# Kernel optimization log

Measured on AMD Instinct MI355X. Metric: run time of the kernel, lower is better.

Reference implementation:

```python
import jax, jax.numpy as jnp
import numpy as np

B = 256       # decode batch
V = 50257     # per-model vocab size (GPT-2-class)
U = 65536     # union vocab size
M = 3         # number of ensembled models


def setup_inputs() -> dict:
    key = jax.random.key(0)
    ks = jax.random.split(key, 7)
    d = {}
    for i in range(M):
        d[f"logits{i}"] = jax.random.normal(ks[i], (B, V), dtype=jnp.float32)
    for i in range(M):
        # vocab_to_token_id mapping: model-local vocab index -> union vocab index
        d[f"map{i}"] = jax.random.randint(ks[M + i], (V,), 0, U, dtype=jnp.int32)
    d["weights"] = jnp.array([0.4, 0.35, 0.25], dtype=jnp.float32)
    return d


def reference(logits0, logits1, logits2, map0, map1, map2, weights):
    # union_probs[b, map_m[j]] += w_m * softmax(logits_m)[b, j]
    union = jnp.zeros((logits0.shape[0], U), dtype=logits0.dtype)
    for m, (lg, mp) in enumerate(zip((logits0, logits1, logits2),
                                     (map0, map1, map2))):
        p = jax.nn.softmax(lg, axis=-1)          # [B, V]
        union = union.at[:, mp].add(weights[m] * p)  # weighted scatter-add into [B, U]
    return union
```

## Files before the change

kernel.cpp:

```cpp
#include <hip/hip_runtime.h>

#define BB 256
#define VV 50257
#define UU 65536
#define MM 3
#define TILE 16
#define NT 4096

typedef float float4a __attribute__((ext_vector_type(4), aligned(4)));

#define WS_Z      0
#define WS_HIST   3072
#define WS_OFF    19456
#define WS_CURSOR 35856
#define WS_SORTED 52240
#define WS_ET     655360
#define WS_NEED   77850112ull

__global__ __launch_bounds__(512) void row_sums_kernel(
    const float* __restrict__ l0, const float* __restrict__ l1,
    const float* __restrict__ l2, const float* __restrict__ weights,
    float* __restrict__ winv)
{
    const int bx = blockIdx.x;
    const int m  = bx >> 8;
    const int b  = bx & 255;
    const float* lg  = (m == 0) ? l0 : (m == 1) ? l1 : l2;
    const float* row = lg + (size_t)b * VV;
    const float4a* rowv = (const float4a*)row;

    const int nv4 = VV / 4;
    float partial = 0.0f;
    for (int i = threadIdx.x; i < nv4; i += 512) {
        float4a v = rowv[i];
        partial += __expf(v.x) + __expf(v.y) + __expf(v.z) + __expf(v.w);
    }
    if (threadIdx.x == 0) partial += __expf(row[VV - 1]);

    #pragma unroll
    for (int off = 32; off > 0; off >>= 1)
        partial += __shfl_down(partial, off, 64);

    __shared__ float smem[8];
    const int lane = threadIdx.x & 63;
    const int wv   = threadIdx.x >> 6;
    if (lane == 0) smem[wv] = partial;
    __syncthreads();
    if (threadIdx.x == 0) {
        float tot = 0.0f;
        #pragma unroll
        for (int w = 0; w < 8; ++w) tot += smem[w];
        winv[bx] = weights[m] / tot;
    }
}

__global__ __launch_bounds__(256) void hist_count_kernel(
    const int* __restrict__ m0, const int* __restrict__ m1,
    const int* __restrict__ m2, int* __restrict__ hist)
{
    const int total = MM * VV;
    for (int idx = blockIdx.x * 256 + threadIdx.x; idx < total;
         idx += gridDim.x * 256) {
        const int m = idx / VV;
        const int j = idx - m * VV;
        const int* mp = (m == 0) ? m0 : (m == 1) ? m1 : m2;
        atomicAdd(&hist[mp[j] >> 4], 1);
    }
}

__global__ __launch_bounds__(1024) void prefix_kernel(
    const int* __restrict__ hist, int* __restrict__ off, int* __restrict__ cursor)
{
    __shared__ int s[1024];
    const int t = threadIdx.x;
    const int4 h = ((const int4*)hist)[t];
    const int sum = h.x + h.y + h.z + h.w;
    s[t] = sum;
    __syncthreads();
    for (int d = 1; d < 1024; d <<= 1) {
        int v = (t >= d) ? s[t - d] : 0;
        __syncthreads();
        s[t] += v;
        __syncthreads();
    }
    const int excl = s[t] - sum;
    int4 o;
    o.x = excl;
    o.y = o.x + h.x;
    o.z = o.y + h.y;
    o.w = o.z + h.z;
    ((int4*)off)[t]    = o;
    ((int4*)cursor)[t] = o;
    if (t == 1023) off[NT] = o.w + h.w;
}

__global__ __launch_bounds__(256) void sort_kernel(
    const int* __restrict__ m0, const int* __restrict__ m1,
    const int* __restrict__ m2, int* __restrict__ cursor,
    int* __restrict__ sorted)
{
    const int total = MM * VV;
    for (int idx = blockIdx.x * 256 + threadIdx.x; idx < total;
         idx += gridDim.x * 256) {
        const int m = idx / VV;
        const int j = idx - m * VV;
        const int* mp = (m == 0) ? m0 : (m == 1) ? m1 : m2;
        const int u = mp[j];
        const int pos = atomicAdd(&cursor[u >> 4], 1);
        sorted[pos] = (j << 8) | (m << 6) | (u & 15);
    }
}

__global__ __launch_bounds__(256) void transpose_exp_kernel(
    const float* __restrict__ l0, const float* __restrict__ l1,
    const float* __restrict__ l2, _Float16* __restrict__ ET,
    float* __restrict__ Z)
{
    const int m  = blockIdx.z;
    const float* lg = (m == 0) ? l0 : (m == 1) ? l1 : l2;
    const int j0 = blockIdx.x * 64;
    const int b0 = blockIdx.y * 64;
    __shared__ float tile[64][65];
    __shared__ float ps[4][64];
    const int lane = threadIdx.x & 63;
    const int sub  = threadIdx.x >> 6;

    const int j = j0 + lane;
    if (j < VV) {
        #pragma unroll
        for (int rr = 0; rr < 16; ++rr) {
            const int b = b0 + rr * 4 + sub;
            tile[lane][rr * 4 + sub] = __expf(lg[(size_t)b * VV + j]);
        }
    }
    __syncthreads();
    float partial = 0.0f;
    #pragma unroll
    for (int rr = 0; rr < 16; ++rr) {
        const int jj = rr * 4 + sub;
        const int jw = j0 + jj;
        if (jw < VV) {
            const float v = tile[jj][lane];
            ET[((size_t)m * VV + jw) * BB + b0 + lane] = (_Float16)v;
            partial += v;
        }
    }
    ps[sub][lane] = partial;
    __syncthreads();
    if (sub == 0)
        atomicAdd(&Z[m * BB + b0 + lane],
                  ps[0][lane] + ps[1][lane] + ps[2][lane] + ps[3][lane]);
}

__global__ __launch_bounds__(256, 8) void accumulate3_kernel(
    const _Float16* __restrict__ ET, const int* __restrict__ sorted,
    const int* __restrict__ off, const float* __restrict__ Z,
    const float* __restrict__ weights, float* __restrict__ out)
{
    const int k = blockIdx.x;
    const int t = threadIdx.x;

    __shared__ float acc[TILE * 256];
    #pragma unroll
    for (int i = 0; i < TILE; ++i) acc[i * 256 + t] = 0.0f;
    const float w0 = weights[0] / Z[0 * BB + t];
    const float w1 = weights[1] / Z[1 * BB + t];
    const float w2 = weights[2] / Z[2 * BB + t];
    __syncthreads();

    const int s = off[k], e = off[k + 1];
    int i = s;
    for (; i + 8 <= e; i += 8) {
        int p[8];
        #pragma unroll
        for (int z = 0; z < 8; ++z) p[z] = sorted[i + z];
        float ev[8];
        #pragma unroll
        for (int z = 0; z < 8; ++z) {
            const int eoff = ((((p[z] >> 6) & 3) * VV + (p[z] >> 8)) << 8);
            ev[z] = (float)ET[eoff + t];
        }
        #pragma unroll
        for (int z = 0; z < 8; ++z) {
            const int ul = p[z] & 15;
            const int m  = (p[z] >> 6) & 3;
            const float w = (m == 0) ? w0 : (m == 1) ? w1 : w2;
            acc[ul * 256 + (t ^ (2 * ul))] += w * ev[z];
        }
    }
    for (; i < e; ++i) {
        const int p = sorted[i];
        const int ul = p & 15;
        const int m  = (p >> 6) & 3;
        const int eoff = (((m * VV) + (p >> 8)) << 8);
        const float w = (m == 0) ? w0 : (m == 1) ? w1 : w2;
        acc[ul * 256 + (t ^ (2 * ul))] += w * (float)ET[eoff + t];
    }
    __syncthreads();

    const int u0   = k * TILE;
    const int slot = t & 15;
    const int q    = t >> 4;
    #pragma unroll
    for (int r = 0; r < 16; ++r) {
        const int b = r * 16 + q;
        out[(size_t)b * UU + u0 + slot] = acc[slot * 256 + (b ^ (2 * slot))];
    }
}

#define FB_NBUCK 8
#define FB_BSZ   8192

__global__ __launch_bounds__(256) void fb_count_kernel(
    const int* __restrict__ m0, const int* __restrict__ m1,
    const int* __restrict__ m2, int* __restrict__ cnt)
{
    const int m = blockIdx.y;
    const int* mp = (m == 0) ? m0 : (m == 1) ? m1 : m2;
    __shared__ int hist[FB_NBUCK];
    if (threadIdx.x < FB_NBUCK) hist[threadIdx.x] = 0;
    __syncthreads();
    const int j = blockIdx.x * 256 + threadIdx.x;
    if (j < VV) atomicAdd(&hist[mp[j] >> 13], 1);
    __syncthreads();
    if (threadIdx.x < FB_NBUCK)
        atomicAdd(&cnt[m * FB_NBUCK + threadIdx.x], hist[threadIdx.x]);
}

__global__ void fb_prefix_kernel(const int* __restrict__ cnt,
                                 int* __restrict__ off, int* __restrict__ cursor)
{
    for (int m = 0; m < MM; ++m) {
        int acc = 0;
        for (int k = 0; k < FB_NBUCK; ++k) {
            off[m * (FB_NBUCK + 1) + k] = acc;
            cursor[m * FB_NBUCK + k]    = acc;
            acc += cnt[m * FB_NBUCK + k];
        }
        off[m * (FB_NBUCK + 1) + FB_NBUCK] = acc;
    }
}

__global__ __launch_bounds__(256) void fb_scatter_kernel(
    const int* __restrict__ m0, const int* __restrict__ m1,
    const int* __restrict__ m2, int* __restrict__ cursor,
    int* __restrict__ sorted)
{
    const int m = blockIdx.y;
    const int* mp = (m == 0) ? m0 : (m == 1) ? m1 : m2;
    int* srt = sorted + (size_t)m * VV;
    const int j = blockIdx.x * 256 + threadIdx.x;
    int u = 0, bucket = FB_NBUCK;
    if (j < VV) { u = mp[j]; bucket = u >> 13; }
    const int lane = threadIdx.x & 63;
    const unsigned long long lt = (1ull << lane) - 1ull;
    #pragma unroll
    for (int k = 0; k < FB_NBUCK; ++k) {
        unsigned long long mask = __ballot(bucket == k);
        if (mask) {
            int leader = __ffsll((long long)mask) - 1;
            int base = 0;
            if (lane == leader)
                base = atomicAdd(&cursor[m * FB_NBUCK + k], __popcll(mask));
            base = __shfl(base, leader, 64);
            if (bucket == k) {
                int pos = base + __popcll(mask & lt);
                srt[pos] = ((u & (FB_BSZ - 1)) << 16) | j;
            }
        }
    }
}

__global__ __launch_bounds__(512) void fb_accumulate_kernel(
    const float* __restrict__ l0, const float* __restrict__ l1,
    const float* __restrict__ l2,
    const int* __restrict__ sorted, const int* __restrict__ off,
    const float* __restrict__ winv, float* __restrict__ out)
{
    const int k = blockIdx.x;
    const int b = blockIdx.y;
    __shared__ float acc[FB_BSZ];
    for (int i = threadIdx.x; i < FB_BSZ; i += 512) acc[i] = 0.0f;
    __syncthreads();
    #pragma unroll
    for (int m = 0; m < MM; ++m) {
        const float* lg = (m == 0) ? l0 : (m == 1) ? l1 : l2;
        const float* row = lg + (size_t)b * VV;
        const int* srt = sorted + (size_t)m * VV;
        const float wv = winv[m * BB + b];
        const int s = off[m * (FB_NBUCK + 1) + k];
        const int e = off[m * (FB_NBUCK + 1) + k + 1];
        for (int i = s + threadIdx.x; i < e; i += 512) {
            const int pack = srt[i];
            atomicAdd(&acc[pack >> 16], wv * __expf(row[pack & 0xFFFF]));
        }
    }
    __syncthreads();
    float* orow = out + (size_t)b * UU + (size_t)k * FB_BSZ;
    for (int i = threadIdx.x; i < FB_BSZ; i += 512) orow[i] = acc[i];
}

extern "C" void kernel_launch(void* const* d_in, const int* in_sizes, int n_in,
                              void* d_out, int out_size, void* d_ws, size_t ws_size,
                              hipStream_t stream)
{
    const float* l0 = (const float*)d_in[0];
    const float* l1 = (const float*)d_in[1];
    const float* l2 = (const float*)d_in[2];
    const int*   m0 = (const int*)d_in[3];
    const int*   m1 = (const int*)d_in[4];
    const int*   m2 = (const int*)d_in[5];
    const float* w  = (const float*)d_in[6];
    float* out = (float*)d_out;
    char* ws = (char*)d_ws;

    if (ws_size >= WS_NEED) {
        float*    Z      = (float*)   (ws + WS_Z);
        int*      hist   = (int*)     (ws + WS_HIST);
        int*      off    = (int*)     (ws + WS_OFF);
        int*      cursor = (int*)     (ws + WS_CURSOR);
        int*      sorted = (int*)     (ws + WS_SORTED);
        _Float16* ET     = (_Float16*)(ws + WS_ET);

        hipMemsetAsync(ws, 0, WS_OFF, stream);

        hist_count_kernel<<<256, 256, 0, stream>>>(m0, m1, m2, hist);
        prefix_kernel<<<1, 1024, 0, stream>>>(hist, off, cursor);
        sort_kernel<<<256, 256, 0, stream>>>(m0, m1, m2, cursor, sorted);

        dim3 gtr((VV + 63) / 64, BB / 64, MM);
        transpose_exp_kernel<<<gtr, 256, 0, stream>>>(l0, l1, l2, ET, Z);

        accumulate3_kernel<<<NT, 256, 0, stream>>>(ET, sorted, off, Z, w, out);
    } else {
        float* winv   = (float*)(ws + 0);
        int*   cnt    = (int*)  (ws + 3072);
        int*   off    = (int*)  (ws + 3200);
        int*   cursor = (int*)  (ws + 3456);
        int*   sorted = (int*)  (ws + 3584);

        hipMemsetAsync(cnt, 0, MM * FB_NBUCK * sizeof(int), stream);
        row_sums_kernel<<<MM * BB, 512, 0, stream>>>(l0, l1, l2, w, winv);
        dim3 gmap((VV + 255) / 256, MM);
        fb_count_kernel<<<gmap, 256, 0, stream>>>(m0, m1, m2, cnt);
        fb_prefix_kernel<<<1, 1, 0, stream>>>(cnt, off, cursor);
        fb_scatter_kernel<<<gmap, 256, 0, stream>>>(m0, m1, m2, cursor, sorted);
        dim3 gacc(FB_NBUCK, BB);
        fb_accumulate_kernel<<<gacc, 512, 0, stream>>>(l0, l1, l2, sorted, off, winv, out);
    }
}
```

Baseline: 287.6 us.

## Restructure exp-transpose to full-batch blocks with vector loads and shuffle scan

The exp/transpose kernel now processes all 256 batch rows per 64-column vocab tile. It uses 4-wide float loads, stores into an fp16 shared tile, and writes ET rows with 8-byte stores, computing row sums with wave shuffles plus atomics. The prefix scan is replaced by a wave-shuffle two-level scan to cut barriers. The aim is to improve memory throughput of the dominant transpose pass, at the cost of unaligned vector loads (the rows have odd length) and more Z atomics.

```diff
diff --git a/kernel.cpp b/kernel.cpp
--- a/kernel.cpp
+++ b/kernel.cpp
@@ -8,6 +8,7 @@
 #define NT 4096
 
 typedef float float4a __attribute__((ext_vector_type(4), aligned(4)));
+typedef _Float16 half4v __attribute__((ext_vector_type(4)));
 
 #define WS_Z      0
 #define WS_HIST   3072
@@ -71,19 +72,34 @@
 __global__ __launch_bounds__(1024) void prefix_kernel(
     const int* __restrict__ hist, int* __restrict__ off, int* __restrict__ cursor)
 {
-    __shared__ int s[1024];
+    __shared__ int wsum[16];
     const int t = threadIdx.x;
+    const int l = t & 63, wv = t >> 6;
     const int4 h = ((const int4*)hist)[t];
     const int sum = h.x + h.y + h.z + h.w;
-    s[t] = sum;
-    __syncthreads();
-    for (int d = 1; d < 1024; d <<= 1) {
-        int v = (t >= d) ? s[t - d] : 0;
-        __syncthreads();
-        s[t] += v;
-        __syncthreads();
-    }
-    const int excl = s[t] - sum;
+
+    int sc = sum;
+    #pragma unroll
+    for (int d = 1; d < 64; d <<= 1) {
+        const int v = __shfl_up(sc, d, 64);
+        if (l >= d) sc += v;
+    }
+    if (l == 63) wsum[wv] = sc;
+    __syncthreads();
+    if (t < 16) {
+        const int ws = wsum[t];
+        int wsc = ws;
+        #pragma unroll
+        for (int d = 1; d < 16; d <<= 1) {
+            const int v = __shfl_up(wsc, d, 64);
+            if (t >= d) wsc += v;
+        }
+        wsum[t] = wsc - ws;
+        if (t == 15) off[NT] = wsc;
+    }
+    __syncthreads();
+
+    const int excl = wsum[wv] + (sc - sum);
     int4 o;
     o.x = excl;
     o.y = o.x + h.x;
@@ -91,7 +107,6 @@
     o.w = o.z + h.z;
     ((int4*)off)[t]    = o;
     ((int4*)cursor)[t] = o;
-    if (t == 1023) off[NT] = o.w + h.w;
 }
 
 __global__ __launch_bounds__(256) void sort_kernel(
@@ -111,45 +126,77 @@
     }
 }
 
-__global__ __launch_bounds__(256) void transpose_exp_kernel(
+__global__ __launch_bounds__(256) void transpose_exp2_kernel(
     const float* __restrict__ l0, const float* __restrict__ l1,
     const float* __restrict__ l2, _Float16* __restrict__ ET,
     float* __restrict__ Z)
 {
-    const int m  = blockIdx.z;
+    const int m  = blockIdx.y;
     const float* lg = (m == 0) ? l0 : (m == 1) ? l1 : l2;
     const int j0 = blockIdx.x * 64;
-    const int b0 = blockIdx.y * 64;
-    __shared__ float tile[64][65];
-    __shared__ float ps[4][64];
-    const int lane = threadIdx.x & 63;
-    const int sub  = threadIdx.x >> 6;
-
-    const int j = j0 + lane;
-    if (j < VV) {
-        #pragma unroll
-        for (int rr = 0; rr < 16; ++rr) {
-            const int b = b0 + rr * 4 + sub;
-            tile[lane][rr * 4 + sub] = __expf(lg[(size_t)b * VV + j]);
-        }
-    }
-    __syncthreads();
-    float partial = 0.0f;
-    #pragma unroll
-    for (int rr = 0; rr < 16; ++rr) {
-        const int jj = rr * 4 + sub;
+
+    __shared__ _Float16 tile[64][258];
+
+    const int t = threadIdx.x;
+    const int l = t & 63;
+    const int g = t & 15;
+    const int r = t >> 4;
+
+    const bool fullj = (j0 + 63) < VV;
+
+    for (int sp = 0; sp < 4; ++sp) {
+        const int bb = r * 16 + sp * 4;
+        float e[4][4];
+        if (fullj) {
+            #pragma unroll
+            for (int q = 0; q < 4; ++q) {
+                const float4a v =
+                    *(const float4a*)(lg + (size_t)(bb + q) * VV + j0 + 4 * g);
+                e[q][0] = __expf(v.x); e[q][1] = __expf(v.y);
+                e[q][2] = __expf(v.z); e[q][3] = __expf(v.w);
+            }
+        } else {
+            #pragma unroll
+            for (int q = 0; q < 4; ++q) {
+                #pragma unroll
+                for (int c = 0; c < 4; ++c) {
+                    const int jc = j0 + 4 * g + c;
+                    e[q][c] = (jc < VV)
+                        ? __expf(lg[(size_t)(bb + q) * VV + jc]) : 0.0f;
+                }
+            }
+        }
+        #pragma unroll
+        for (int c = 0; c < 4; ++c) {
+            half4v hv;
+            hv.x = (_Float16)e[0][c];
+            hv.y = (_Float16)e[1][c];
+            hv.z = (_Float16)e[2][c];
+            hv.w = (_Float16)e[3][c];
+            *(half4v*)&tile[4 * g + c][bb] = hv;
+        }
+        #pragma unroll
+        for (int q = 0; q < 4; ++q) {
+            float s = (e[q][0] + e[q][1]) + (e[q][2] + e[q][3]);
+            s += __shfl_xor(s, 1, 64);
+            s += __shfl_xor(s, 2, 64);
+            s += __shfl_xor(s, 4, 64);
+            s += __shfl_xor(s, 8, 64);
+            if (g == 0) atomicAdd(&Z[m * BB + bb + q], s);
+        }
+    }
+    __syncthreads();
+
+    const int wv = t >> 6;
+    #pragma unroll
+    for (int it = 0; it < 16; ++it) {
+        const int jj = wv * 16 + it;
         const int jw = j0 + jj;
         if (jw < VV) {
-            const float v = tile[jj][lane];
-            ET[((size_t)m * VV + jw) * BB + b0 + lane] = (_Float16)v;
-            partial += v;
-        }
-    }
-    ps[sub][lane] = partial;
-    __syncthreads();
-    if (sub == 0)
-        atomicAdd(&Z[m * BB + b0 + lane],
-                  ps[0][lane] + ps[1][lane] + ps[2][lane] + ps[3][lane]);
+            const uint2 d = *(const uint2*)&tile[jj][4 * l];
+            *(uint2*)(ET + ((size_t)m * VV + jw) * BB + 4 * l) = d;
+        }
+    }
 }
 
 __global__ __launch_bounds__(256, 8) void accumulate3_kernel(
@@ -328,8 +375,8 @@
         prefix_kernel<<<1, 1024, 0, stream>>>(hist, off, cursor);
         sort_kernel<<<256, 256, 0, stream>>>(m0, m1, m2, cursor, sorted);
 
-        dim3 gtr((VV + 63) / 64, BB / 64, MM);
-        transpose_exp_kernel<<<gtr, 256, 0, stream>>>(l0, l1, l2, ET, Z);
+        dim3 gtr((VV + 63) / 64, MM);
+        transpose_exp2_kernel<<<gtr, 256, 0, stream>>>(l0, l1, l2, ET, Z);
 
         accumulate3_kernel<<<NT, 256, 0, stream>>>(ET, sorted, off, Z, w, out);
     } else {
```

After: 686.3 us. 2.39x slower.
